# Optimization experiments

Hardware: AMD Instinct MI355X
Metric: run time of the kernel (lower is better)

The kernel has to match this reference:

```python
import jax, jax.numpy as jnp
import numpy as np

GAMMA = 1.0
BIG = 1e30  # finite stand-in for +inf (safe under logsumexp and autodiff)


def setup_inputs() -> dict:
    key = jax.random.key(0)
    kx, ky = jax.random.split(key)
    x = jax.random.normal(kx, (32, 512, 64), dtype=jnp.float32)
    y = jax.random.normal(ky, (32, 512, 64), dtype=jnp.float32)
    return {"x": x, "y": y}


def _cosine_dist(x, y):
    # 1 - cosine similarity; matches F.normalize(p=2, eps=1e-12)
    xn = x / jnp.maximum(jnp.linalg.norm(x, axis=-1, keepdims=True), 1e-12)
    yn = y / jnp.maximum(jnp.linalg.norm(y, axis=-1, keepdims=True), 1e-12)
    return 1.0 - jnp.einsum('btd,bsd->bts', xn, yn)


def _soft_dtw(D, gamma):
    # Anti-diagonal soft-DTW DP. D: [B, T1, T2] -> [B]
    B, T1, T2 = D.shape
    R0 = jnp.full((B, T1 + 1, T2 + 1), BIG, dtype=D.dtype).at[:, 0, 0].set(0.0)
    i = jnp.arange(1, T1 + 1)  # all rows; each diagonal k has j = k - i

    def step(R, k):
        j = k - i
        valid = (j >= 1) & (j <= T2)
        jc = jnp.where(valid, j, 0)  # clamp invalid lanes; masked below
        cost = jnp.where(valid, D[:, i - 1, jnp.clip(jc - 1, 0, T2 - 1)], 0.0)
        r_diag = R[:, i - 1, jnp.clip(jc - 1, 0, T2)]
        r_left = R[:, i, jnp.clip(jc - 1, 0, T2)]
        r_up = R[:, i - 1, jc]
        stacked = jnp.stack([r_diag, r_left, r_up], axis=0)  # [3, B, T1]
        stacked = jnp.where(valid[None, None, :], stacked, 0.0)
        soft_min = -gamma * jax.nn.logsumexp(-stacked / gamma, axis=0)
        new = cost + soft_min
        old = R[:, i, jc]
        R = R.at[:, i, jc].set(jnp.where(valid[None, :], new, old))
        return R, None

    ks = jnp.arange(2, T1 + T2 + 1)
    R, _ = jax.lax.scan(step, R0, ks)
    return R[:, T1, T2]


def reference(x, y):
    D_xy = _cosine_dist(x, y)
    D_xx = _cosine_dist(x, x)
    D_yy = _cosine_dist(y, y)
    sdtw_xy = _soft_dtw(D_xy, GAMMA)
    sdtw_xx = _soft_dtw(D_xx, GAMMA)
    sdtw_yy = _soft_dtw(D_yy, GAMMA)
    return sdtw_xy - 0.5 * (sdtw_xx + sdtw_yy)
```

## Files before the change

kernel.cpp:

```cpp
#include <hip/hip_runtime.h>
#include <hip/hip_fp16.h>

#define T1 512
#define NB 32
#define NP 96
#define DHEAD 64

#define RSLOTS 128
#define RBYTES (RSLOTS * 1024)
#define PFD 24

typedef __attribute__((ext_vector_type(8))) short bf16x8;
typedef __attribute__((ext_vector_type(4))) float f32x4;
typedef __attribute__((ext_vector_type(4))) unsigned int u32x4;

__global__ __launch_bounds__(256) void k_normalize(const float* __restrict__ x,
                                                   const float* __restrict__ y,
                                                   ushort* __restrict__ xb,
                                                   ushort* __restrict__ yb) {
  int wid  = threadIdx.x >> 6;
  int lane = threadIdx.x & 63;
  int row  = blockIdx.x * 4 + wid;
  const float* src; ushort* dst;
  if (row < NB * T1) { src = x + (size_t)row * DHEAD;            dst = xb + (size_t)row * DHEAD; }
  else { int r2 = row - NB * T1; src = y + (size_t)r2 * DHEAD;   dst = yb + (size_t)r2 * DHEAD; }
  float v = src[lane];
  float s = v * v;
  #pragma unroll
  for (int off = 32; off > 0; off >>= 1) s += __shfl_xor(s, off);
  float rn = 1.0f / fmaxf(sqrtf(s), 1e-12f);
  float o = v * rn;
  unsigned u = __float_as_uint(o);
  unsigned r = (u + 0x7fffu + ((u >> 16) & 1u)) >> 16;
  dst[lane] = (ushort)r;
}

__global__ __launch_bounds__(256) void k_gemm_w(const ushort* __restrict__ xb,
                                                const ushort* __restrict__ yb,
                                                __half* __restrict__ W) {
  int pb = blockIdx.z;
  int p  = pb >> 5;
  int b  = pb & 31;
  const ushort* A  = ((p == 2) ? yb : xb) + (size_t)b * T1 * DHEAD;
  const ushort* Bm = ((p == 1) ? xb : yb) + (size_t)b * T1 * DHEAD;

  int wid = threadIdx.x >> 6, lane = threadIdx.x & 63;
  int wm = wid >> 1, wn = wid & 1;
  int i0 = blockIdx.x * 128 + wm * 64;
  int j0 = blockIdx.y * 128 + wn * 64;
  int lr = lane & 15, kg = lane >> 4;

  f32x4 acc[4][4];
  #pragma unroll
  for (int ic = 0; ic < 4; ++ic)
    #pragma unroll
    for (int jc = 0; jc < 4; ++jc) acc[ic][jc] = (f32x4){0.f, 0.f, 0.f, 0.f};

  #pragma unroll
  for (int kk = 0; kk < 2; ++kk) {
    int ko = kk * 32 + kg * 8;
    bf16x8 af[4], bf[4];
    #pragma unroll
    for (int ic = 0; ic < 4; ++ic)
      af[ic] = *reinterpret_cast<const bf16x8*>(A + (size_t)(i0 + ic * 16 + lr) * DHEAD + ko);
    #pragma unroll
    for (int jc = 0; jc < 4; ++jc)
      bf[jc] = *reinterpret_cast<const bf16x8*>(Bm + (size_t)(j0 + jc * 16 + lr) * DHEAD + ko);
    #pragma unroll
    for (int ic = 0; ic < 4; ++ic)
      #pragma unroll
      for (int jc = 0; jc < 4; ++jc)
        acc[ic][jc] = __builtin_amdgcn_mfma_f32_16x16x32_bf16(af[ic], bf[jc], acc[ic][jc], 0, 0, 0);
  }

  const float NLOG2E = -1.44269504088896340736f;
  __half* Wp = W + (size_t)pb * (T1 * T1);
  int ib = kg << 2;
  #pragma unroll
  for (int ic = 0; ic < 4; ++ic) {
    int i = i0 + ic * 16 + ib;
    #pragma unroll
    for (int jc = 0; jc < 4; ++jc) {
      int j = j0 + jc * 16 + lr;
      union { __half h[4]; uint2 u; } pk;
      #pragma unroll
      for (int r = 0; r < 4; ++r) {
        float d = 1.0f - acc[ic][jc][r];
        pk.h[r] = __float2half(exp2f(NLOG2E * d));
      }
      *reinterpret_cast<uint2*>(Wp + (size_t)j * T1 + i) = pk.u;
    }
  }
}

__global__ __launch_bounds__(64, 1) void k_dtw(const __half* __restrict__ W,
                                               float* __restrict__ res) {
  __shared__ __attribute__((aligned(16))) char ring[RBYTES];
  const int prob = blockIdx.x;
  const __half* Wp = W + (size_t)prob * (T1 * T1);
  const int lane = threadIdx.x;

  float Va[8], Vb[8];
  #pragma unroll
  for (int r = 0; r < 8; ++r) { Va[r] = 0.f; Vb[r] = 0.f; }
  float B2 = 0.f, B2p = 0.f;
  const float dgSeed = (lane == 0) ? 1.0f : 0.0f;

  auto dppshr = [](float v) -> float {
    return __int_as_float(__builtin_amdgcn_update_dpp(
        0, __float_as_int(v), 0x138 , 0xF, 0xF, true));
  };

  auto issueLoad = [&](int c) {
    int cc = c > T1 - 1 ? T1 - 1 : c;
    const __half* gp = Wp + ((size_t)cc << 9) + (lane << 3);
    char* lp = &ring[(cc & (RSLOTS - 1)) << 10];
    __builtin_amdgcn_global_load_lds(
        (const __attribute__((address_space(1))) void*)gp,
        (__attribute__((address_space(3))) void*)lp, 16, 0, 0);
  };

  auto readSlot = [&](int t) -> u32x4 {
    int j = t - lane;
    return *reinterpret_cast<const u32x4*>(
        &ring[((j & (RSLOTS - 1)) << 10) + (lane << 4)]);
  };

#define DTW_STEP(kk, VIN, VOUT, SDG, INJSEED) do {                            \
    const int t_ = tb + (kk);                                                 \
    float nbUp_ = dppshr(VIN[7]);                    \
    float nbDg_ = dppshr(VOUT[7]);                   \
    float up_ = nbUp_ * sUp;                                                  \
    float dg_ = nbDg_ * (SDG);                                                \
    if (INJSEED) dg_ = dgSeed;                     \
    union { u32x4 u; __half h[8]; } cv_; cv_.u = d0;                          \
    float wv_[8];                                                             \
    _Pragma("unroll")                                                         \
    for (int r = 0; r < 8; ++r) wv_[r] = __half2float(cv_.h[r]);              \
    d0 = d1; d1 = d2; d2 = readSlot(t_ + 3);                                  \
    issueLoad(t_ + PFD);                                                      \
    int j_ = t_ - lane;                                                       \
    if ((unsigned)j_ < (unsigned)T1) {                                        \
      float c_ = fmaf(wv_[0], up_, wv_[0] * (dg_ + VIN[0]));                  \
      VOUT[0] = c_;                                                           \
      _Pragma("unroll")                                                       \
      for (int r = 1; r < 8; ++r) {                                           \
        c_ = fmaf(wv_[r], c_, wv_[r] * (VIN[r-1] + VIN[r]));                  \
        VOUT[r] = c_;                                                         \
      }                                                                       \
      if ((kk) == 7) {                        \
        float m_ = fmaxf(fmaxf(fmaxf(VOUT[0],VOUT[1]),fmaxf(VOUT[2],VOUT[3])),\
                         fmaxf(fmaxf(VOUT[4],VOUT[5]),fmaxf(VOUT[6],VOUT[7])));\
        int e_ = (int)((__float_as_uint(m_) >> 23) & 0xFF) - 127;             \
        e_ = e_ < -126 ? -126 : (e_ > 126 ? 126 : e_);                        \
        float sc_ = __uint_as_float((unsigned)(127 - e_) << 23);              \
        _Pragma("unroll")                                                     \
        for (int r = 0; r < 8; ++r) VOUT[r] *= sc_;                           \
        B2p = B2; B2 -= (float)e_;                                            \
      }                                                                       \
    }                                                                         \
  } while (0)

#define DTW_GROUP(SEEDFLAG) do {                                              \
    asm volatile("s_waitcnt vmcnt(13)" ::: "memory");   \
    float nbBn_ = dppshr(B2);                 \
    float nbBo_ = dppshr(B2p);                \
    int du_ = (int)fminf(fmaxf(B2 - nbBn_, -120.f), 120.f);                   \
    int dd_ = (int)fminf(fmaxf(B2 - nbBo_, -120.f), 120.f);                   \
    float sUp  = __uint_as_float((unsigned)(127 + du_) << 23);      \
    float sDg0 = __uint_as_float((unsigned)(127 + dd_) << 23);      \
    DTW_STEP(0, Va, Vb, sDg0, SEEDFLAG);                                      \
    DTW_STEP(1, Vb, Va, sUp, false);                                          \
    DTW_STEP(2, Va, Vb, sUp, false);                                          \
    DTW_STEP(3, Vb, Va, sUp, false);                                          \
    DTW_STEP(4, Va, Vb, sUp, false);                                          \
    DTW_STEP(5, Vb, Va, sUp, false);                                          \
    DTW_STEP(6, Va, Vb, sUp, false);                                          \
    DTW_STEP(7, Vb, Va, sUp, false);                                          \
  } while (0)

  #pragma unroll
  for (int c = 0; c < PFD; ++c) issueLoad(c);
  asm volatile("s_waitcnt vmcnt(21)" ::: "memory");
  u32x4 d0 = readSlot(0), d1 = readSlot(1), d2 = readSlot(2);

  { const int tb = 0; DTW_GROUP(true); }
  for (int tb = 8; tb < 576; tb += 8) DTW_GROUP(false);

  if (lane == 63) {
    res[prob] = (B2 - log2f(Va[7])) * 0.69314718055994530942f;
  }
#undef DTW_STEP
#undef DTW_GROUP
}

__global__ void k_combine(const float* __restrict__ res, float* __restrict__ out) {
  int b = threadIdx.x;
  if (b < NB) out[b] = res[b] - 0.5f * (res[NB + b] + res[2 * NB + b]);
}

extern "C" void kernel_launch(void* const* d_in, const int* in_sizes, int n_in,
                              void* d_out, int out_size, void* d_ws, size_t ws_size,
                              hipStream_t stream) {
  const float* x = (const float*)d_in[0];
  const float* y = (const float*)d_in[1];
  float* out = (float*)d_out;

  const size_t xb_off  = 0;
  const size_t yb_off  = (size_t)NB * T1 * DHEAD * sizeof(ushort);
  const size_t W_off   = 2 * yb_off;
  const size_t res_off = W_off + (size_t)3 * NB * T1 * T1 * sizeof(__half);
  const size_t need    = res_off + NP * sizeof(float);

  if (ws_size < need) {
    hipMemsetAsync(d_out, 0xFF, (size_t)out_size * sizeof(float), stream);
    return;
  }

  ushort* xb  = (ushort*)((char*)d_ws + xb_off);
  ushort* yb  = (ushort*)((char*)d_ws + yb_off);
  __half* W   = (__half*)((char*)d_ws + W_off);
  float*  res = (float*)((char*)d_ws + res_off);

  hipLaunchKernelGGL(k_normalize, dim3(8192), dim3(256), 0, stream, x, y, xb, yb);
  hipLaunchKernelGGL(k_gemm_w, dim3(4, 4, 96), dim3(256), 0, stream, xb, yb, W);
  hipLaunchKernelGGL(k_dtw, dim3(NP), dim3(64), 0, stream, W, res);
  hipLaunchKernelGGL(k_combine, dim3(1), dim3(64), 0, stream, res, out);
}
```

Baseline: 101.6 us.

## Deepen LDS prefetch ring, unroll slot reads, and drop bounds guard in steady state

Raises the global-to-LDS prefetch depth and replaces the rolling three-register slot window with eight register slots read eight steps ahead, using incrementally updated LDS and global addresses instead of recomputing them each step. The main diagonal loop is split so the per-lane bounds check runs only in the head and tail groups, and the steady-state groups run unguarded. The aim is to cut per-step address arithmetic and branching and to hide more memory latency in this serial, latency-bound DP. The cost is more registers and relying on the correctness of the split loop bounds.

New measurement: 92.18 us. 9.3% less time.

```diff
diff --git a/kernel.cpp b/kernel.cpp
--- a/kernel.cpp
+++ b/kernel.cpp
@@ -8,7 +8,7 @@
 
 #define RSLOTS 128
 #define RBYTES (RSLOTS * 1024)
-#define PFD 24
+#define PFD 32
 
 typedef __attribute__((ext_vector_type(8))) short bf16x8;
 typedef __attribute__((ext_vector_type(4))) float f32x4;
@@ -111,36 +111,50 @@
         0, __float_as_int(v), 0x138 , 0xF, 0xF, true));
   };
 
-  auto issueLoad = [&](int c) {
-    int cc = c > T1 - 1 ? T1 - 1 : c;
-    const __half* gp = Wp + ((size_t)cc << 9) + (lane << 3);
-    char* lp = &ring[(cc & (RSLOTS - 1)) << 10];
+  const char* gsrc = (const char*)Wp + (size_t)PFD * 1024 + (lane << 4);
+  unsigned lslot = (PFD << 10) & (RBYTES - 1);
+
+  #pragma unroll
+  for (int c = 0; c < PFD; ++c) {
+    const __half* gp = Wp + ((size_t)c << 9) + (lane << 3);
     __builtin_amdgcn_global_load_lds(
         (const __attribute__((address_space(1))) void*)gp,
-        (__attribute__((address_space(3))) void*)lp, 16, 0, 0);
-  };
-
-  auto readSlot = [&](int t) -> u32x4 {
-    int j = t - lane;
-    return *reinterpret_cast<const u32x4*>(
-        &ring[((j & (RSLOTS - 1)) << 10) + (lane << 4)]);
-  };
-
-#define DTW_STEP(kk, VIN, VOUT, SDG, INJSEED) do {                            \
-    const int t_ = tb + (kk);                                                 \
+        (__attribute__((address_space(3))) void*)(ring + ((unsigned)(c << 10))), 16, 0, 0);
+  }
+  asm volatile("s_waitcnt vmcnt(24)" ::: "memory");
+
+  u32x4 d0, d1, d2, d3, d4, d5, d6, d7;
+  unsigned va0, va1, va2, va3, va4, va5, va6, va7;
+#define RS_INIT(K) do { \
+    d##K = *reinterpret_cast<const u32x4*>( \
+        ring + ((((unsigned)(K - lane) & 127u) << 10) | (unsigned)(lane << 4))); \
+    va##K = ((((unsigned)(8 + K - lane) & 127u) << 10) | (unsigned)(lane << 4)); \
+  } while (0)
+  RS_INIT(0); RS_INIT(1); RS_INIT(2); RS_INIT(3);
+  RS_INIT(4); RS_INIT(5); RS_INIT(6); RS_INIT(7);
+#undef RS_INIT
+
+#define DTW_STEP(KK, VIN, VOUT, SDG, SEEDK, GUARD) do {                       \
+    const int t_ = tb + (KK);                                                 \
     float nbUp_ = dppshr(VIN[7]);                    \
     float nbDg_ = dppshr(VOUT[7]);                   \
     float up_ = nbUp_ * sUp;                                                  \
     float dg_ = nbDg_ * (SDG);                                                \
-    if (INJSEED) dg_ = dgSeed;                     \
-    union { u32x4 u; __half h[8]; } cv_; cv_.u = d0;                          \
+    if (SEEDK) dg_ = dgSeed;                                                  \
+    union { u32x4 u; __half h[8]; } cv_; cv_.u = d##KK;                       \
+    d##KK = *reinterpret_cast<const u32x4*>(ring + va##KK);     \
+    va##KK = (va##KK + 8192u) & (RBYTES - 1);                                 \
+    __builtin_amdgcn_global_load_lds(                          \
+        (const __attribute__((address_space(1))) void*)gsrc,                  \
+        (__attribute__((address_space(3))) void*)(ring + lslot), 16, 0, 0);   \
+    lslot = (lslot + 1024u) & (RBYTES - 1);                                   \
+    gsrc += ((t_ + PFD) < T1 - 1) ? 1024 : 0;           \
     float wv_[8];                                                             \
     _Pragma("unroll")                                                         \
     for (int r = 0; r < 8; ++r) wv_[r] = __half2float(cv_.h[r]);              \
-    d0 = d1; d1 = d2; d2 = readSlot(t_ + 3);                                  \
-    issueLoad(t_ + PFD);                                                      \
-    int j_ = t_ - lane;                                                       \
-    if ((unsigned)j_ < (unsigned)T1) {                                        \
+    bool act_ = true;                                                         \
+    if (GUARD) { int j_ = t_ - lane; act_ = ((unsigned)j_ < (unsigned)T1); }  \
+    if (act_) {                                                               \
       float c_ = fmaf(wv_[0], up_, wv_[0] * (dg_ + VIN[0]));                  \
       VOUT[0] = c_;                                                           \
       _Pragma("unroll")                                                       \
@@ -148,7 +162,7 @@
         c_ = fmaf(wv_[r], c_, wv_[r] * (VIN[r-1] + VIN[r]));                  \
         VOUT[r] = c_;                                                         \
       }                                                                       \
-      if ((kk) == 7) {                        \
+      if ((KK) == 7) {                                 \
         float m_ = fmaxf(fmaxf(fmaxf(VOUT[0],VOUT[1]),fmaxf(VOUT[2],VOUT[3])),\
                          fmaxf(fmaxf(VOUT[4],VOUT[5]),fmaxf(VOUT[6],VOUT[7])));\
         int e_ = (int)((__float_as_uint(m_) >> 23) & 0xFF) - 127;             \
@@ -161,31 +175,30 @@
     }                                                                         \
   } while (0)
 
-#define DTW_GROUP(SEEDFLAG) do {                                              \
-    asm volatile("s_waitcnt vmcnt(13)" ::: "memory");   \
+#define DTW_GROUP(GUARD, SEED) do {                                           \
+    asm volatile("s_waitcnt vmcnt(16)" ::: "memory");      \
     float nbBn_ = dppshr(B2);                 \
     float nbBo_ = dppshr(B2p);                \
-    int du_ = (int)fminf(fmaxf(B2 - nbBn_, -120.f), 120.f);                   \
-    int dd_ = (int)fminf(fmaxf(B2 - nbBo_, -120.f), 120.f);                   \
-    float sUp  = __uint_as_float((unsigned)(127 + du_) << 23);      \
-    float sDg0 = __uint_as_float((unsigned)(127 + dd_) << 23);      \
-    DTW_STEP(0, Va, Vb, sDg0, SEEDFLAG);                                      \
-    DTW_STEP(1, Vb, Va, sUp, false);                                          \
-    DTW_STEP(2, Va, Vb, sUp, false);                                          \
-    DTW_STEP(3, Vb, Va, sUp, false);                                          \
-    DTW_STEP(4, Va, Vb, sUp, false);                                          \
-    DTW_STEP(5, Vb, Va, sUp, false);                                          \
-    DTW_STEP(6, Va, Vb, sUp, false);                                          \
-    DTW_STEP(7, Vb, Va, sUp, false);                                          \
+    float sUp  = __uint_as_float(                                             \
+        (unsigned)(127 + (int)fminf(fmaxf(B2 - nbBn_, -120.f), 120.f)) << 23);\
+    float sDg0 = __uint_as_float(                                             \
+        (unsigned)(127 + (int)fminf(fmaxf(B2 - nbBo_, -120.f), 120.f)) << 23);\
+    DTW_STEP(0, Va, Vb, sDg0, SEED, GUARD);                                   \
+    DTW_STEP(1, Vb, Va, sUp, false, GUARD);                                   \
+    DTW_STEP(2, Va, Vb, sUp, false, GUARD);                                   \
+    DTW_STEP(3, Vb, Va, sUp, false, GUARD);                                   \
+    DTW_STEP(4, Va, Vb, sUp, false, GUARD);                                   \
+    DTW_STEP(5, Vb, Va, sUp, false, GUARD);                                   \
+    DTW_STEP(6, Va, Vb, sUp, false, GUARD);                                   \
+    DTW_STEP(7, Vb, Va, sUp, false, GUARD);                                   \
   } while (0)
 
-  #pragma unroll
-  for (int c = 0; c < PFD; ++c) issueLoad(c);
-  asm volatile("s_waitcnt vmcnt(21)" ::: "memory");
-  u32x4 d0 = readSlot(0), d1 = readSlot(1), d2 = readSlot(2);
-
-  { const int tb = 0; DTW_GROUP(true); }
-  for (int tb = 8; tb < 576; tb += 8) DTW_GROUP(false);
+  { const int tb = 0; DTW_GROUP(true, true); }
+  #pragma unroll 1
+  for (int tb = 8; tb < 64; tb += 8)  DTW_GROUP(true, false);
+  #pragma unroll 1
+  for (int tb = 64; tb < 568; tb += 8) DTW_GROUP(false, false);
+  { const int tb = 568; DTW_GROUP(true, false); }
 
   if (lane == 63) {
     res[prob] = (B2 - log2f(Va[7])) * 0.69314718055994530942f;
```
